# Kernel optimization log

Measured on AMD Instinct MI355X. Metric: run time of the kernel, lower is better.

Reference implementation:

```python
import jax, jax.numpy as jnp
import numpy as np

DIM = 768
HEADS = 12
HEAD_DIM = DIM // HEADS
MAX_LEN = 2048
EPS = 1e-5

def layer_norm(x, w, b):
    mu = jnp.mean(x, axis=-1, keepdims=True)
    var = jnp.var(x, axis=-1, keepdims=True)
    return (x - mu) * jax.lax.rsqrt(var + EPS) * w + b


def setup_inputs() -> dict:
    key = jax.random.key(0)
    ks = jax.random.split(key, 16)
    B, N = 2, 2048
    s = 1.0 / np.sqrt(DIM)
    inp = {
        "visible_features": jax.random.normal(ks[0], (B, N, DIM), jnp.float32),
        "infrared_features": jax.random.normal(ks[1], (B, N, DIM), jnp.float32),
        "wq": jax.random.normal(ks[2], (DIM, DIM), jnp.float32) * s,
        "bq": jnp.zeros((DIM,), jnp.float32),
        "lnq_w": jnp.ones((DIM,), jnp.float32),
        "lnq_b": jnp.zeros((DIM,), jnp.float32),
        "wk": jax.random.normal(ks[3], (DIM, DIM), jnp.float32) * s,
        "bk": jnp.zeros((DIM,), jnp.float32),
        "lnk_w": jnp.ones((DIM,), jnp.float32),
        "lnk_b": jnp.zeros((DIM,), jnp.float32),
        "wv": jax.random.normal(ks[4], (DIM, DIM), jnp.float32) * s,
        "bv": jnp.zeros((DIM,), jnp.float32),
        "lnv_w": jnp.ones((DIM,), jnp.float32),
        "lnv_b": jnp.zeros((DIM,), jnp.float32),
        "pos_emb": jax.random.normal(ks[5], (MAX_LEN, DIM), jnp.float32),
        "wo": jax.random.normal(ks[6], (DIM, DIM), jnp.float32) * s,
        "bo": jnp.zeros((DIM,), jnp.float32),
        "gate_w": jax.random.normal(ks[7], (DIM, 2 * DIM), jnp.float32) * (1.0 / np.sqrt(2 * DIM)),
        "gate_b": jnp.zeros((DIM,), jnp.float32),
        "ln_w": jnp.ones((DIM,), jnp.float32),
        "ln_b": jnp.zeros((DIM,), jnp.float32),
    }
    return inp


def reference(visible_features, infrared_features, wq, bq, lnq_w, lnq_b,
              wk, bk, lnk_w, lnk_b, wv, bv, lnv_w, lnv_b,
              pos_emb, wo, bo, gate_w, gate_b, ln_w, ln_b):
    B, N, _ = visible_features.shape
    scale = HEAD_DIM ** -0.5

    def proj_heads(x, w, b, gw, gb):
        y = layer_norm(x @ w.T + b, gw, gb)  # [B,N,D]
        return y.reshape(B, N, HEADS, HEAD_DIM).transpose(0, 2, 1, 3)  # [B,H,N,d]

    q = proj_heads(infrared_features, wq, bq, lnq_w, lnq_b)
    k = proj_heads(visible_features, wk, bk, lnk_w, lnk_b)
    v = proj_heads(visible_features, wv, bv, lnv_w, lnv_b)

    pos = pos_emb[:N].reshape(1, N, HEADS, HEAD_DIM).transpose(0, 2, 1, 3)  # [1,H,N,d]

    scores = jnp.einsum('bhnd,bhmd->bhnm', q, k) * scale
    scores = scores + jnp.einsum('bhnd,xhmd->bhnm', q, pos)
    attn = jax.nn.softmax(scores, axis=-1)  # dropout is identity in eval

    out = jnp.einsum('bhnm,bhmd->bhnd', attn, v)
    out = out.transpose(0, 2, 1, 3).reshape(B, N, DIM)
    out = out @ wo.T + bo

    gate = jax.nn.sigmoid(jnp.concatenate([visible_features, out], axis=-1) @ gate_w.T + gate_b)
    fused = visible_features * gate + out * (1.0 - gate)
    return layer_norm(fused, ln_w, ln_b)
```

## Files before the change

### kernel.cpp

```cpp
#include <hip/hip_runtime.h>
#include <hip/hip_bf16.h>

#define DIMC 768
#define NSEQ 2048
#define NB 2
#define NH 12
#define HD 64
#define EPSLN 1e-5f
#define LOG2E 1.44269504f

typedef __attribute__((ext_vector_type(8))) short          bf16x8;
typedef __attribute__((ext_vector_type(8))) unsigned short ushort8;
typedef __attribute__((ext_vector_type(4))) unsigned short ushort4v;
typedef __attribute__((ext_vector_type(4))) float          f32x4;
typedef __attribute__((ext_vector_type(2))) unsigned int   u32x2;
typedef unsigned int u32;

__device__ __forceinline__ unsigned short f2b(float f) {
    union { float f; unsigned u; } x; x.f = f;
    unsigned r = x.u + 0x7fffu + ((x.u >> 16) & 1u);
    return (unsigned short)(r >> 16);
}
__device__ __forceinline__ float b2f(unsigned short v) {
    union { unsigned u; float f; } x; x.u = ((u32)v) << 16; return x.f;
}

#define MFMA16(a, b, c) __builtin_amdgcn_mfma_f32_16x16x32_bf16((a), (b), (c), 0, 0, 0)

__device__ __forceinline__ void gl_lds16(const unsigned short* g, unsigned short* l) {
    __builtin_amdgcn_global_load_lds(
        (const __attribute__((address_space(1))) u32*)(const void*)g,
        (__attribute__((address_space(3))) u32*)(void*)l, 16, 0, 0);
}

#define G_WQ   147456
#define G_MW   442368
#define G_G2   147456
#define G_WO   147456
#define G_VIS  786432
#define G_INF  786432
#define G_BF_TOTAL (G_WQ + G_MW + G_G2 + G_WO + G_VIS + G_INF)
#define G_BIAS 576
#define G_ALL  (G_BF_TOTAL + G_BIAS)

__global__ __launch_bounds__(256)
void cast_all_kernel(const float* __restrict__ wq, const float* __restrict__ wk,
                     const float* __restrict__ wv, const float* __restrict__ gw,
                     const float* __restrict__ wo,
                     const float* __restrict__ bk, const float* __restrict__ bv,
                     const float* __restrict__ gb,
                     const float* __restrict__ vis, const float* __restrict__ inf_,
                     unsigned short* __restrict__ o_wq, unsigned short* __restrict__ o_mw,
                     unsigned short* __restrict__ o_g2, unsigned short* __restrict__ o_wo,
                     unsigned short* __restrict__ o_wot,
                     unsigned short* __restrict__ o_vis, unsigned short* __restrict__ o_inf,
                     float* __restrict__ o_biasc)
{
    const int g = blockIdx.x * 256 + threadIdx.x;
    if (g >= G_ALL) return;
    if (g >= G_BF_TOTAL) {
        const int e0 = (g - G_BF_TOTAL) * 4;
        float4 r;
        float* pr = (float*)&r;
        #pragma unroll
        for (int t = 0; t < 4; ++t) {
            const int e = e0 + t;
            pr[t] = (e < 768) ? bk[e] : (e < 1536) ? bv[e - 768] : gb[e - 1536];
        }
        *(float4*)&o_biasc[e0] = r;
        return;
    }
    const float* src; unsigned short* dst; int soff, doff = 0;
    bool is_wo = false; int wor = 0, woc = 0;
    int gg = g;
    if (gg < G_WQ) { src = wq; dst = o_wq; soff = gg; doff = gg; }
    else if ((gg -= G_WQ) < G_MW) {
        const int row = gg / 192, c4 = gg % 192;
        dst = o_mw; doff = gg;
        if      (row < 768)  { src = wk; soff = row * 192 + c4; }
        else if (row < 1536) { src = wv; soff = (row - 768) * 192 + c4; }
        else                 { src = gw; soff = (row - 1536) * 384 + c4; }
    }
    else if ((gg -= G_MW) < G_G2) {
        const int row = gg / 192, c4 = gg % 192;
        src = gw; soff = row * 384 + 192 + c4; dst = o_g2; doff = gg;
    }
    else if ((gg -= G_G2) < G_WO) {
        src = wo; dst = o_wo; soff = gg; doff = gg;
        is_wo = true; wor = gg / 192; woc = (gg % 192) * 4;
    }
    else if ((gg -= G_WO) < G_VIS) { src = vis;  dst = o_vis; soff = gg; doff = gg; }
    else { gg -= G_VIS;              src = inf_; dst = o_inf; soff = gg; doff = gg; }
    f32x4 v = ((const f32x4*)src)[soff];
    ushort4v t;
    t[0] = f2b(v[0]); t[1] = f2b(v[1]); t[2] = f2b(v[2]); t[3] = f2b(v[3]);
    ((ushort4v*)dst)[doff] = t;
    if (is_wo) {
        #pragma unroll
        for (int e = 0; e < 4; ++e)
            o_wot[(size_t)(woc + e) * DIMC + wor] = t[e];
    }
}

__global__ __launch_bounds__(256)
void bias2_kernel(const float* __restrict__ gw, const float* __restrict__ bo,
                  float* __restrict__ biasc2)
{
    const int i = blockIdx.x * 256 + threadIdx.x;
    if (i >= 768) return;
    biasc2[i] = bo[i];
    const float* row = gw + (size_t)i * 1536 + 768;
    float s = 0.f;
    for (int k = 0; k < 768; k += 4) {
        float4 gv = *(const float4*)&row[k];
        float4 bv = *(const float4*)&bo[k];
        s += gv.x * bv.x + gv.y * bv.y + gv.z * bv.z + gv.w * bv.w;
    }
    biasc2[768 + i] = s;
}

__device__ __forceinline__ void gemm_core128(const unsigned short* __restrict__ A,
                                             const unsigned short* __restrict__ W,
                                             int m0, int n0,
                                             unsigned short* As, unsigned short* Bs,
                                             f32x4 (&acc)[4][4])
{
    const int lane = threadIdx.x & 63, wid = threadIdx.x >> 6;
    const int wm = wid >> 1, wn = wid & 1;
    const int r16 = lane & 15, kg = lane >> 4;
    const int lr = lane >> 3, lc = (lane & 7) * 8;

    auto stage = [&](int k0, int buf) {
        #pragma unroll
        for (int i = 0; i < 4; ++i) {
            const int c = wid * 4 + i;
            gl_lds16(&A[(size_t)(m0 + c * 8 + lr) * DIMC + k0 + lc], &As[buf * 8192 + c * 512]);
            gl_lds16(&W[(size_t)(n0 + c * 8 + lr) * DIMC + k0 + lc], &Bs[buf * 8192 + c * 512]);
        }
    };

    stage(0, 0);
    for (int t = 0; t < 12; ++t) {
        const int cur = t & 1;
        if (t < 11) {
            stage((t + 1) * 64, cur ^ 1);
            asm volatile("s_waitcnt vmcnt(8)" ::: "memory");
        } else {
            asm volatile("s_waitcnt vmcnt(0)" ::: "memory");
        }
        __builtin_amdgcn_s_barrier();
        __builtin_amdgcn_sched_barrier(0);
        #pragma unroll
        for (int ks = 0; ks < 2; ++ks) {
            bf16x8 af[4], bg[4];
            #pragma unroll
            for (int mi = 0; mi < 4; ++mi)
                af[mi] = *(const bf16x8*)&As[cur * 8192 + (wm * 64 + mi * 16 + r16) * 64 + ks * 32 + kg * 8];
            #pragma unroll
            for (int nj = 0; nj < 4; ++nj)
                bg[nj] = *(const bf16x8*)&Bs[cur * 8192 + (wn * 64 + nj * 16 + r16) * 64 + ks * 32 + kg * 8];
            __builtin_amdgcn_s_setprio(1);
            #pragma unroll
            for (int mi = 0; mi < 4; ++mi)
                #pragma unroll
                for (int nj = 0; nj < 4; ++nj)
                    acc[mi][nj] = MFMA16(af[mi], bg[nj], acc[mi][nj]);
            __builtin_amdgcn_s_setprio(0);
        }
        __builtin_amdgcn_sched_barrier(0);
        __builtin_amdgcn_s_barrier();
    }
}

__global__ __launch_bounds__(256)
void gemm_p1(const unsigned short* __restrict__ inf_b, const unsigned short* __restrict__ vis_b,
             const unsigned short* __restrict__ g2_b,  const unsigned short* __restrict__ wq_b,
             const unsigned short* __restrict__ mw_b,  const unsigned short* __restrict__ wo_t,
             const float* __restrict__ bq, const float* __restrict__ biasc,
             unsigned short* __restrict__ qpre,
             unsigned short* __restrict__ k_b, unsigned short* __restrict__ v_b,
             float* __restrict__ Gd, unsigned short* __restrict__ W2)
{
    __shared__ unsigned short As[2 * 8192];
    __shared__ unsigned short Bs[2 * 8192];
    const int orig = (int)blockIdx.x;
    const int xcd = orig & 7, ix = orig >> 3;
    int bid = (xcd < 4 ? xcd * 101 : 404 + (xcd - 4) * 100) + ix;

    const unsigned short *A, *W;
    int m0, n0, sub;
    if (bid < 192)      { sub = 0; const int b = bid;       m0 = (b / 6)  * 128; n0 = (b % 6)  * 128; A = inf_b; W = wq_b; }
    else if (bid < 768) { sub = 1; const int b = bid - 192; m0 = (b / 18) * 128; n0 = (b % 18) * 128; A = vis_b; W = mw_b; }
    else                { sub = 2; const int b = bid - 768; m0 = (b / 6)  * 128; n0 = (b % 6)  * 128; A = g2_b;  W = wo_t; }

    f32x4 acc[4][4] = {};
    gemm_core128(A, W, m0, n0, As, Bs, acc);

    const int lane = threadIdx.x & 63, wid = threadIdx.x >> 6;
    const int wm = wid >> 1, wn = wid & 1;
    const int r16 = lane & 15, kg = lane >> 4;
    #pragma unroll
    for (int mi = 0; mi < 4; ++mi)
    #pragma unroll
    for (int nj = 0; nj < 4; ++nj) {
        const int gr0 = m0 + wm * 64 + mi * 16 + kg * 4;
        const int gc  = n0 + wn * 64 + nj * 16 + r16;
        #pragma unroll
        for (int r = 0; r < 4; ++r) {
            const int gr = gr0 + r;
            float val = acc[mi][nj][r];
            if (sub == 0) {
                qpre[(size_t)gr * DIMC + gc] = f2b(val + bq[gc]);
            } else if (sub == 1) {
                val += biasc[gc];
                if      (gc < 768)  k_b[(size_t)gr * DIMC + gc] = f2b(val);
                else if (gc < 1536) v_b[(size_t)gr * DIMC + (gc - 768)] = f2b(val);
                else                Gd[(size_t)gr * DIMC + (gc - 1536)] = val;
            } else {
                W2[(size_t)gr * DIMC + gc] = f2b(val);
            }
        }
    }
}

__global__ __launch_bounds__(256)
void gemm_p2(const unsigned short* __restrict__ ao_b, const unsigned short* __restrict__ wo_cat,
             const float* __restrict__ biasc2,
             float* __restrict__ Oc, float* __restrict__ Gd)
{
    __shared__ unsigned short As[2 * 8192];
    __shared__ unsigned short Bs[2 * 8192];
    int bid = (int)blockIdx.x;
    bid = (bid & 7) * 48 + (bid >> 3);
    const int m0 = (bid / 12) * 128, n0 = (bid % 12) * 128;

    f32x4 acc[4][4] = {};
    gemm_core128(ao_b, wo_cat, m0, n0, As, Bs, acc);

    const int lane = threadIdx.x & 63, wid = threadIdx.x >> 6;
    const int wm = wid >> 1, wn = wid & 1;
    const int r16 = lane & 15, kg = lane >> 4;
    #pragma unroll
    for (int mi = 0; mi < 4; ++mi)
    #pragma unroll
    for (int nj = 0; nj < 4; ++nj) {
        const int gr0 = m0 + wm * 64 + mi * 16 + kg * 4;
        const int gc  = n0 + wn * 64 + nj * 16 + r16;
        #pragma unroll
        for (int r = 0; r < 4; ++r) {
            const int gr = gr0 + r;
            const float val = acc[mi][nj][r] + biasc2[gc];
            if (gc < 768) Oc[(size_t)gr * DIMC + gc] = val;
            else          Gd[(size_t)gr * DIMC + (gc - 768)] += val;
        }
    }
}

__global__ __launch_bounds__(256)
void ln_all_kernel(const unsigned short* __restrict__ qpre,
                   const float* __restrict__ lnqw, const float* __restrict__ lnqb,
                   const float* __restrict__ lnkw, const float* __restrict__ lnkb,
                   const float* __restrict__ lnvw, const float* __restrict__ lnvb,
                   const float* __restrict__ pos,
                   unsigned short* __restrict__ q_b,
                   unsigned short* __restrict__ k_b, unsigned short* __restrict__ v_b)
{
    const int bid = blockIdx.x;
    const int mode = bid >> 12;
    const int row = bid & 4095;
    const int n = row & (NSEQ - 1);
    const unsigned short* src;
    unsigned short* dst;
    const float *w, *b;
    if (mode == 0)      { src = qpre + (size_t)row * DIMC; dst = q_b + (size_t)row * DIMC; w = lnqw; b = lnqb; }
    else if (mode == 1) { src = dst = k_b + (size_t)row * DIMC; w = lnkw; b = lnkb; }
    else                { src = dst = v_b + (size_t)row * DIMC; w = lnvw; b = lnvb; }

    float x[3];
    float s = 0.f, q = 0.f;
    #pragma unroll
    for (int u = 0; u < 3; ++u) {
        const int j = threadIdx.x + u * 256;
        x[u] = b2f(src[j]);
        s += x[u];
        q += x[u] * x[u];
    }
    #pragma unroll
    for (int off = 32; off > 0; off >>= 1) {
        s += __shfl_down(s, off);
        q += __shfl_down(q, off);
    }
    __shared__ float ls[8];
    const int wv_ = threadIdx.x >> 6;
    if ((threadIdx.x & 63) == 0) { ls[wv_] = s; ls[4 + wv_] = q; }
    __syncthreads();
    if (threadIdx.x == 0) {
        ls[0] = ls[0] + ls[1] + ls[2] + ls[3];
        ls[4] = ls[4] + ls[5] + ls[6] + ls[7];
    }
    __syncthreads();
    const float mu  = ls[0] * (1.f / DIMC);
    const float var = ls[4] * (1.f / DIMC) - mu * mu;
    const float rs  = rsqrtf(var + EPSLN);
    #pragma unroll
    for (int u = 0; u < 3; ++u) {
        const int j = threadIdx.x + u * 256;
        float y = (x[u] - mu) * rs * w[j] + b[j];
        if (mode == 1) y = y * (0.125f * LOG2E) + pos[(size_t)n * DIMC + j] * LOG2E;
        dst[j] = f2b(y);
    }
}

__global__ __launch_bounds__(256, 3)
void attn_bf16_kernel(const unsigned short* __restrict__ Q,
                      const unsigned short* __restrict__ K,
                      const unsigned short* __restrict__ V,
                      unsigned short* __restrict__ O)
{
    __shared__ unsigned short Ks[128][72];
    __shared__ unsigned short Vt[64][136];
    __shared__ unsigned short Ps[4][16][136];

    const int bh = blockIdx.x;
    const int b = bh / NH, h = bh % NH;
    const int n0 = blockIdx.y * 64;
    const int tid = threadIdx.x;
    const int lane = tid & 63, w = tid >> 6;
    const int r16 = lane & 15, kg = lane >> 4;

    const size_t base = (size_t)b * NSEQ * DIMC + (size_t)h * HD;

    const size_t qoff = base + (size_t)(n0 + w * 16 + r16) * DIMC + kg * 8;
    bf16x8 aq0 = *(const bf16x8*)&Q[qoff];
    bf16x8 aq1 = *(const bf16x8*)&Q[qoff + 32];

    const int krow = tid >> 1;
    const int kcol = (tid & 1) * 32;
    const unsigned short* Kg = K + base + (size_t)krow * DIMC + kcol;
    const int vkv = lane;
    const int vdc = w * 16;
    const unsigned short* Vg = V + base + (size_t)vkv * DIMC + vdc;

    f32x4 o[4] = {};
    float m_run = -1e30f, l_run = 0.f;

    ushort8 pk[4];
    ushort8 pv[2][2];

    auto pf_load = [&](size_t adv) {
        #pragma unroll
        for (int i = 0; i < 4; ++i) pk[i] = *(const ushort8*)(Kg + adv + 8 * i);
        #pragma unroll
        for (int rep = 0; rep < 2; ++rep)
            #pragma unroll
            for (int hh = 0; hh < 2; ++hh)
                pv[rep][hh] = *(const ushort8*)(Vg + adv + (size_t)rep * 64 * DIMC + hh * 8);
    };
    auto pf_write = [&]() {
        #pragma unroll
        for (int i = 0; i < 4; ++i) *(ushort8*)&Ks[krow][kcol + 8 * i] = pk[i];
        #pragma unroll
        for (int rep = 0; rep < 2; ++rep)
            #pragma unroll
            for (int hh = 0; hh < 2; ++hh)
                #pragma unroll
                for (int e = 0; e < 8; ++e)
                    Vt[vdc + hh * 8 + e][vkv + rep * 64] = pv[rep][hh][e];
    };

    pf_load(0);
    pf_write();
    __syncthreads();

    for (int m0 = 0; m0 < NSEQ; m0 += 128) {
        const bool more = (m0 + 128 < NSEQ);
        if (more) pf_load((size_t)(m0 + 128) * DIMC);
        __builtin_amdgcn_sched_barrier(0);

        f32x4 sv[8];
        #pragma unroll
        for (int f = 0; f < 8; ++f) sv[f] = (f32x4){0.f, 0.f, 0.f, 0.f};
        __builtin_amdgcn_s_setprio(1);
        #pragma unroll
        for (int f = 0; f < 8; ++f) {
            bf16x8 kb0 = *(const bf16x8*)&Ks[f * 16 + r16][kg * 8];
            bf16x8 kb1 = *(const bf16x8*)&Ks[f * 16 + r16][32 + kg * 8];
            sv[f] = MFMA16(kb0, aq0, sv[f]);
            sv[f] = MFMA16(kb1, aq1, sv[f]);
        }
        __builtin_amdgcn_s_setprio(0);

        float mf[8];
        #pragma unroll
        for (int f = 0; f < 8; ++f)
            mf[f] = fmaxf(fmaxf(sv[f][0], sv[f][1]), fmaxf(sv[f][2], sv[f][3]));
        float m01 = fmaxf(mf[0], mf[1]), m23 = fmaxf(mf[2], mf[3]);
        float m45 = fmaxf(mf[4], mf[5]), m67 = fmaxf(mf[6], mf[7]);
        float mt = fmaxf(fmaxf(m01, m23), fmaxf(m45, m67));
        mt = fmaxf(mt, __shfl_xor(mt, 16));
        mt = fmaxf(mt, __shfl_xor(mt, 32));

        const bool defer = __all(mt - m_run <= 8.0f);
        float corr = 1.f;
        if (!defer) {
            const float mn = fmaxf(m_run, mt);
            corr = exp2f(m_run - mn);
            m_run = mn;
        }

        float sf[8];
        #pragma unroll
        for (int f = 0; f < 8; ++f) {
            float p0 = exp2f(sv[f][0] - m_run);
            float p1 = exp2f(sv[f][1] - m_run);
            float p2 = exp2f(sv[f][2] - m_run);
            float p3 = exp2f(sv[f][3] - m_run);
            sf[f] = (p0 + p1) + (p2 + p3);
            u32 w0, w1;
            asm("v_cvt_pk_bf16_f32 %0, %1, %2" : "=v"(w0) : "v"(p0), "v"(p1));
            asm("v_cvt_pk_bf16_f32 %0, %1, %2" : "=v"(w1) : "v"(p2), "v"(p3));
            u32x2 pw; pw[0] = w0; pw[1] = w1;
            *(u32x2*)&Ps[w][r16][f * 16 + kg * 4] = pw;
        }
        float st = ((sf[0] + sf[1]) + (sf[2] + sf[3])) + ((sf[4] + sf[5]) + (sf[6] + sf[7]));
        st += __shfl_xor(st, 16);
        st += __shfl_xor(st, 32);
        l_run = l_run * corr + st;

        if (!defer) {
            #pragma unroll
            for (int jj = 0; jj < 4; ++jj) {
                const float cq = __shfl(corr, kg * 4 + jj);
                o[0][jj] *= cq; o[1][jj] *= cq; o[2][jj] *= cq; o[3][jj] *= cq;
            }
        }

        bf16x8 pa[4];
        #pragma unroll
        for (int s = 0; s < 4; ++s)
            pa[s] = *(const bf16x8*)&Ps[w][r16][s * 32 + kg * 8];
        __builtin_amdgcn_s_setprio(1);
        #pragma unroll
        for (int nj = 0; nj < 4; ++nj) {
            #pragma unroll
            for (int s = 0; s < 4; ++s) {
                bf16x8 vb = *(const bf16x8*)&Vt[nj * 16 + r16][s * 32 + kg * 8];
                o[nj] = MFMA16(pa[s], vb, o[nj]);
            }
        }
        __builtin_amdgcn_s_setprio(0);

        __builtin_amdgcn_s_barrier();
        __builtin_amdgcn_sched_barrier(0);
        if (more) pf_write();
        __syncthreads();
    }

    const float linv = 1.f / l_run;
    #pragma unroll
    for (int jj = 0; jj < 4; ++jj) {
        const float cq = __shfl(linv, kg * 4 + jj);
        #pragma unroll
        for (int nj = 0; nj < 4; ++nj) {
            const size_t go = base + (size_t)(n0 + w * 16 + kg * 4 + jj) * DIMC + nj * 16 + r16;
            O[go] = f2b(o[nj][jj] * cq);
        }
    }
}

__global__ __launch_bounds__(256)
void fuse_ln_kernel(const float* __restrict__ vis,
                    const float* __restrict__ Oc,
                    const float* __restrict__ G,
                    const float* __restrict__ w,
                    const float* __restrict__ b,
                    float* __restrict__ out)
{
    const int row = blockIdx.x;
    float f[3];
    float s = 0.f, q = 0.f;
    #pragma unroll
    for (int u = 0; u < 3; ++u) {
        const size_t idx = (size_t)row * DIMC + threadIdx.x + u * 256;
        const float vv = vis[idx];
        const float oo = Oc[idx];
        const float gg = 1.f / (1.f + __expf(-G[idx]));
        f[u] = vv * gg + oo * (1.f - gg);
        s += f[u];
        q += f[u] * f[u];
    }
    #pragma unroll
    for (int off = 32; off > 0; off >>= 1) {
        s += __shfl_down(s, off);
        q += __shfl_down(q, off);
    }
    __shared__ float ls[8];
    const int wv_ = threadIdx.x >> 6;
    if ((threadIdx.x & 63) == 0) { ls[wv_] = s; ls[4 + wv_] = q; }
    __syncthreads();
    if (threadIdx.x == 0) {
        ls[0] = ls[0] + ls[1] + ls[2] + ls[3];
        ls[4] = ls[4] + ls[5] + ls[6] + ls[7];
    }
    __syncthreads();
    const float mu  = ls[0] * (1.f / DIMC);
    const float var = ls[4] * (1.f / DIMC) - mu * mu;
    const float rs  = rsqrtf(var + EPSLN);
    #pragma unroll
    for (int u = 0; u < 3; ++u) {
        const int j = threadIdx.x + u * 256;
        out[(size_t)row * DIMC + j] = (f[u] - mu) * rs * w[j] + b[j];
    }
}

extern "C" void kernel_launch(void* const* d_in, const int* in_sizes, int n_in,
                              void* d_out, int out_size, void* d_ws, size_t ws_size,
                              hipStream_t stream)
{
    const float* vis  = (const float*)d_in[0];
    const float* inf_ = (const float*)d_in[1];
    const float* wq   = (const float*)d_in[2];
    const float* bq   = (const float*)d_in[3];
    const float* lnqw = (const float*)d_in[4];
    const float* lnqb = (const float*)d_in[5];
    const float* wk   = (const float*)d_in[6];
    const float* bk   = (const float*)d_in[7];
    const float* lnkw = (const float*)d_in[8];
    const float* lnkb = (const float*)d_in[9];
    const float* wv   = (const float*)d_in[10];
    const float* bv   = (const float*)d_in[11];
    const float* lnvw = (const float*)d_in[12];
    const float* lnvb = (const float*)d_in[13];
    const float* pos  = (const float*)d_in[14];
    const float* wo   = (const float*)d_in[15];
    const float* bo   = (const float*)d_in[16];
    const float* gw   = (const float*)d_in[17];
    const float* gb   = (const float*)d_in[18];
    const float* lnw  = (const float*)d_in[19];
    const float* lnb  = (const float*)d_in[20];

    const size_t WEL = 589824;
    const size_t MWEL = 1769472;
    const size_t BUF = (size_t)NB * NSEQ * DIMC;

    unsigned short* p = (unsigned short*)d_ws;
    unsigned short* wq_b   = p;  p += WEL;
    unsigned short* mw_b   = p;  p += MWEL;
    unsigned short* g2_b   = p;  p += WEL;
    unsigned short* wo_b   = p;  p += WEL;
    unsigned short* W2     = p;  p += WEL;
    unsigned short* wo_t   = p;  p += WEL;
    unsigned short* vis_b  = p;  p += BUF;
    unsigned short* inf_b  = p;  p += BUF;
    unsigned short* qpre_b = p;  p += BUF;
    unsigned short* q_b    = p;  p += BUF;
    unsigned short* k_b    = p;  p += BUF;
    unsigned short* v_b    = p;  p += BUF;
    float* biasc  = (float*)p;  p += 4608;
    float* biasc2 = (float*)p;  p += 3072;

    float* Gd = (float*)d_out;
    float* Oc = (float*)k_b;

    dim3 blk(256);

    bias2_kernel<<<dim3(3), blk, 0, stream>>>(gw, bo, biasc2);
    cast_all_kernel<<<dim3((G_ALL + 255) / 256), blk, 0, stream>>>(
        wq, wk, wv, gw, wo, bk, bv, gb, vis, inf_,
        wq_b, mw_b, g2_b, wo_b, wo_t, vis_b, inf_b, biasc);

    gemm_p1<<<dim3(804), blk, 0, stream>>>(inf_b, vis_b, g2_b, wq_b, mw_b, wo_t,
                                           bq, biasc, qpre_b, k_b, v_b, Gd, W2);

    ln_all_kernel<<<dim3(12288), blk, 0, stream>>>(qpre_b, lnqw, lnqb, lnkw, lnkb,
                                                   lnvw, lnvb, pos, q_b, k_b, v_b);

    attn_bf16_kernel<<<dim3(NB * NH, NSEQ / 64), blk, 0, stream>>>(q_b, k_b, v_b, q_b);

    gemm_p2<<<dim3(384), blk, 0, stream>>>(q_b, wo_b, biasc2, Oc, Gd);

    fuse_ln_kernel<<<dim3(4096), blk, 0, stream>>>(vis, Oc, Gd, lnw, lnb, (float*)d_out);
}
```

Baseline: 338.3 us.

## Replace precomputed Wo·G2 weight fold with sequential Wo then gate GEMMs

```diff
diff --git a/kernel.cpp b/kernel.cpp
--- a/kernel.cpp
+++ b/kernel.cpp
@@ -52,7 +52,6 @@
                      const float* __restrict__ vis, const float* __restrict__ inf_,
                      unsigned short* __restrict__ o_wq, unsigned short* __restrict__ o_mw,
                      unsigned short* __restrict__ o_g2, unsigned short* __restrict__ o_wo,
-                     unsigned short* __restrict__ o_wot,
                      unsigned short* __restrict__ o_vis, unsigned short* __restrict__ o_inf,
                      float* __restrict__ o_biasc)
 {
@@ -71,7 +70,6 @@
         return;
     }
     const float* src; unsigned short* dst; int soff, doff = 0;
-    bool is_wo = false; int wor = 0, woc = 0;
     int gg = g;
     if (gg < G_WQ) { src = wq; dst = o_wq; soff = gg; doff = gg; }
     else if ((gg -= G_WQ) < G_MW) {
@@ -85,45 +83,20 @@
         const int row = gg / 192, c4 = gg % 192;
         src = gw; soff = row * 384 + 192 + c4; dst = o_g2; doff = gg;
     }
-    else if ((gg -= G_G2) < G_WO) {
-        src = wo; dst = o_wo; soff = gg; doff = gg;
-        is_wo = true; wor = gg / 192; woc = (gg % 192) * 4;
-    }
+    else if ((gg -= G_G2) < G_WO)  { src = wo;   dst = o_wo;  soff = gg; doff = gg; }
     else if ((gg -= G_WO) < G_VIS) { src = vis;  dst = o_vis; soff = gg; doff = gg; }
     else { gg -= G_VIS;              src = inf_; dst = o_inf; soff = gg; doff = gg; }
     f32x4 v = ((const f32x4*)src)[soff];
     ushort4v t;
     t[0] = f2b(v[0]); t[1] = f2b(v[1]); t[2] = f2b(v[2]); t[3] = f2b(v[3]);
     ((ushort4v*)dst)[doff] = t;
-    if (is_wo) {
-        #pragma unroll
-        for (int e = 0; e < 4; ++e)
-            o_wot[(size_t)(woc + e) * DIMC + wor] = t[e];
-    }
-}
-
-__global__ __launch_bounds__(256)
-void bias2_kernel(const float* __restrict__ gw, const float* __restrict__ bo,
-                  float* __restrict__ biasc2)
-{
-    const int i = blockIdx.x * 256 + threadIdx.x;
-    if (i >= 768) return;
-    biasc2[i] = bo[i];
-    const float* row = gw + (size_t)i * 1536 + 768;
-    float s = 0.f;
-    for (int k = 0; k < 768; k += 4) {
-        float4 gv = *(const float4*)&row[k];
-        float4 bv = *(const float4*)&bo[k];
-        s += gv.x * bv.x + gv.y * bv.y + gv.z * bv.z + gv.w * bv.w;
-    }
-    biasc2[768 + i] = s;
-}
-
-__device__ __forceinline__ void gemm_core128(const unsigned short* __restrict__ A,
-                                             const unsigned short* __restrict__ W,
-                                             int m0, int n0,
-                                             unsigned short* As, unsigned short* Bs,
-                                             f32x4 (&acc)[4][4])
+}
+
+__device__ __forceinline__ void gemm_core(const unsigned short* __restrict__ A,
+                                          const unsigned short* __restrict__ W,
+                                          int m0, int n0,
+                                          unsigned short* As, unsigned short* Bs,
+                                          f32x4 (&acc)[4][2])
 {
     const int lane = threadIdx.x & 63, wid = threadIdx.x >> 6;
     const int wm = wid >> 1, wn = wid & 1;
@@ -135,7 +108,11 @@
         for (int i = 0; i < 4; ++i) {
             const int c = wid * 4 + i;
             gl_lds16(&A[(size_t)(m0 + c * 8 + lr) * DIMC + k0 + lc], &As[buf * 8192 + c * 512]);
-            gl_lds16(&W[(size_t)(n0 + c * 8 + lr) * DIMC + k0 + lc], &Bs[buf * 8192 + c * 512]);
+        }
+        #pragma unroll
+        for (int i = 0; i < 2; ++i) {
+            const int c = wid * 2 + i;
+            gl_lds16(&W[(size_t)(n0 + c * 8 + lr) * DIMC + k0 + lc], &Bs[buf * 4096 + c * 512]);
         }
     };
 
@@ -144,7 +121,7 @@
         const int cur = t & 1;
         if (t < 11) {
             stage((t + 1) * 64, cur ^ 1);
-            asm volatile("s_waitcnt vmcnt(8)" ::: "memory");
+            asm volatile("s_waitcnt vmcnt(6)" ::: "memory");
         } else {
             asm volatile("s_waitcnt vmcnt(0)" ::: "memory");
         }
@@ -152,18 +129,18 @@
         __builtin_amdgcn_sched_barrier(0);
         #pragma unroll
         for (int ks = 0; ks < 2; ++ks) {
-            bf16x8 af[4], bg[4];
+            bf16x8 af[4], bg[2];
             #pragma unroll
             for (int mi = 0; mi < 4; ++mi)
                 af[mi] = *(const bf16x8*)&As[cur * 8192 + (wm * 64 + mi * 16 + r16) * 64 + ks * 32 + kg * 8];
             #pragma unroll
-            for (int nj = 0; nj < 4; ++nj)
-                bg[nj] = *(const bf16x8*)&Bs[cur * 8192 + (wn * 64 + nj * 16 + r16) * 64 + ks * 32 + kg * 8];
+            for (int nj = 0; nj < 2; ++nj)
+                bg[nj] = *(const bf16x8*)&Bs[cur * 4096 + (wn * 32 + nj * 16 + r16) * 64 + ks * 32 + kg * 8];
             __builtin_amdgcn_s_setprio(1);
             #pragma unroll
             for (int mi = 0; mi < 4; ++mi)
                 #pragma unroll
-                for (int nj = 0; nj < 4; ++nj)
+                for (int nj = 0; nj < 2; ++nj)
                     acc[mi][nj] = MFMA16(af[mi], bg[nj], acc[mi][nj]);
             __builtin_amdgcn_s_setprio(0);
         }
@@ -174,27 +151,22 @@
 
 __global__ __launch_bounds__(256)
 void gemm_p1(const unsigned short* __restrict__ inf_b, const unsigned short* __restrict__ vis_b,
-             const unsigned short* __restrict__ g2_b,  const unsigned short* __restrict__ wq_b,
-             const unsigned short* __restrict__ mw_b,  const unsigned short* __restrict__ wo_t,
+             const unsigned short* __restrict__ wq_b,  const unsigned short* __restrict__ mw_b,
              const float* __restrict__ bq, const float* __restrict__ biasc,
              unsigned short* __restrict__ qpre,
              unsigned short* __restrict__ k_b, unsigned short* __restrict__ v_b,
-             float* __restrict__ Gd, unsigned short* __restrict__ W2)
+             float* __restrict__ Gd)
 {
     __shared__ unsigned short As[2 * 8192];
-    __shared__ unsigned short Bs[2 * 8192];
-    const int orig = (int)blockIdx.x;
-    const int xcd = orig & 7, ix = orig >> 3;
-    int bid = (xcd < 4 ? xcd * 101 : 404 + (xcd - 4) * 100) + ix;
-
+    __shared__ unsigned short Bs[2 * 4096];
+    const int bid = (int)blockIdx.x;
     const unsigned short *A, *W;
     int m0, n0, sub;
-    if (bid < 192)      { sub = 0; const int b = bid;       m0 = (b / 6)  * 128; n0 = (b % 6)  * 128; A = inf_b; W = wq_b; }
-    else if (bid < 768) { sub = 1; const int b = bid - 192; m0 = (b / 18) * 128; n0 = (b % 18) * 128; A = vis_b; W = mw_b; }
-    else                { sub = 2; const int b = bid - 768; m0 = (b / 6)  * 128; n0 = (b % 6)  * 128; A = g2_b;  W = wo_t; }
-
-    f32x4 acc[4][4] = {};
-    gemm_core128(A, W, m0, n0, As, Bs, acc);
+    if (bid < 384) { sub = 0; const int b = bid;       m0 = (b / 12) * 128; n0 = (b % 12) * 64; A = inf_b; W = wq_b; }
+    else           { sub = 1; const int b = bid - 384; m0 = (b / 36) * 128; n0 = (b % 36) * 64; A = vis_b; W = mw_b; }
+
+    f32x4 acc[4][2] = {};
+    gemm_core(A, W, m0, n0, As, Bs, acc);
 
     const int lane = threadIdx.x & 63, wid = threadIdx.x >> 6;
     const int wm = wid >> 1, wn = wid & 1;
@@ -202,40 +174,37 @@
     #pragma unroll
     for (int mi = 0; mi < 4; ++mi)
     #pragma unroll
-    for (int nj = 0; nj < 4; ++nj) {
+    for (int nj = 0; nj < 2; ++nj) {
         const int gr0 = m0 + wm * 64 + mi * 16 + kg * 4;
-        const int gc  = n0 + wn * 64 + nj * 16 + r16;
+        const int gc  = n0 + wn * 32 + nj * 16 + r16;
         #pragma unroll
         for (int r = 0; r < 4; ++r) {
             const int gr = gr0 + r;
             float val = acc[mi][nj][r];
             if (sub == 0) {
                 qpre[(size_t)gr * DIMC + gc] = f2b(val + bq[gc]);
-            } else if (sub == 1) {
+            } else {
                 val += biasc[gc];
                 if      (gc < 768)  k_b[(size_t)gr * DIMC + gc] = f2b(val);
                 else if (gc < 1536) v_b[(size_t)gr * DIMC + (gc - 768)] = f2b(val);
                 else                Gd[(size_t)gr * DIMC + (gc - 1536)] = val;
-            } else {
-                W2[(size_t)gr * DIMC + gc] = f2b(val);
             }
         }
     }
 }
 
 __global__ __launch_bounds__(256)
-void gemm_p2(const unsigned short* __restrict__ ao_b, const unsigned short* __restrict__ wo_cat,
-             const float* __restrict__ biasc2,
-             float* __restrict__ Oc, float* __restrict__ Gd)
+void gemm_wo(const unsigned short* __restrict__ ao_b, const unsigned short* __restrict__ wo_b,
+             const float* __restrict__ bo,
+             float* __restrict__ Oc, unsigned short* __restrict__ oc_b)
 {
     __shared__ unsigned short As[2 * 8192];
-    __shared__ unsigned short Bs[2 * 8192];
-    int bid = (int)blockIdx.x;
-    bid = (bid & 7) * 48 + (bid >> 3);
-    const int m0 = (bid / 12) * 128, n0 = (bid % 12) * 128;
-
-    f32x4 acc[4][4] = {};
-    gemm_core128(ao_b, wo_cat, m0, n0, As, Bs, acc);
+    __shared__ unsigned short Bs[2 * 4096];
+    const int bid = (int)blockIdx.x;
+    const int m0 = (bid / 12) * 128, n0 = (bid % 12) * 64;
+
+    f32x4 acc[4][2] = {};
+    gemm_core(ao_b, wo_b, m0, n0, As, Bs, acc);
 
     const int lane = threadIdx.x & 63, wid = threadIdx.x >> 6;
     const int wm = wid >> 1, wn = wid & 1;
@@ -243,16 +212,43 @@
     #pragma unroll
     for (int mi = 0; mi < 4; ++mi)
     #pragma unroll
-    for (int nj = 0; nj < 4; ++nj) {
+    for (int nj = 0; nj < 2; ++nj) {
         const int gr0 = m0 + wm * 64 + mi * 16 + kg * 4;
-        const int gc  = n0 + wn * 64 + nj * 16 + r16;
+        const int gc  = n0 + wn * 32 + nj * 16 + r16;
         #pragma unroll
         for (int r = 0; r < 4; ++r) {
-            const int gr = gr0 + r;
-            const float val = acc[mi][nj][r] + biasc2[gc];
-            if (gc < 768) Oc[(size_t)gr * DIMC + gc] = val;
-            else          Gd[(size_t)gr * DIMC + (gc - 768)] += val;
-        }
+            const size_t idx = (size_t)(gr0 + r) * DIMC + gc;
+            const float val = acc[mi][nj][r] + bo[gc];
+            Oc[idx] = val;
+            oc_b[idx] = f2b(val);
+        }
+    }
+}
+
+__global__ __launch_bounds__(256)
+void gemm_g2(const unsigned short* __restrict__ oc_b, const unsigned short* __restrict__ g2_b,
+             float* __restrict__ Gd)
+{
+    __shared__ unsigned short As[2 * 8192];
+    __shared__ unsigned short Bs[2 * 4096];
+    const int bid = (int)blockIdx.x;
+    const int m0 = (bid / 12) * 128, n0 = (bid % 12) * 64;
+
+    f32x4 acc[4][2] = {};
+    gemm_core(oc_b, g2_b, m0, n0, As, Bs, acc);
+
+    const int lane = threadIdx.x & 63, wid = threadIdx.x >> 6;
+    const int wm = wid >> 1, wn = wid & 1;
+    const int r16 = lane & 15, kg = lane >> 4;
+    #pragma unroll
+    for (int mi = 0; mi < 4; ++mi)
+    #pragma unroll
+    for (int nj = 0; nj < 2; ++nj) {
+        const int gr0 = m0 + wm * 64 + mi * 16 + kg * 4;
+        const int gc  = n0 + wn * 32 + nj * 16 + r16;
+        #pragma unroll
+        for (int r = 0; r < 4; ++r)
+            Gd[(size_t)(gr0 + r) * DIMC + gc] += acc[mi][nj][r];
     }
 }
 
@@ -548,36 +544,35 @@
     unsigned short* mw_b   = p;  p += MWEL;
     unsigned short* g2_b   = p;  p += WEL;
     unsigned short* wo_b   = p;  p += WEL;
-    unsigned short* W2     = p;  p += WEL;
-    unsigned short* wo_t   = p;  p += WEL;
     unsigned short* vis_b  = p;  p += BUF;
     unsigned short* inf_b  = p;  p += BUF;
     unsigned short* qpre_b = p;  p += BUF;
     unsigned short* q_b    = p;  p += BUF;
     unsigned short* k_b    = p;  p += BUF;
     unsigned short* v_b    = p;  p += BUF;
-    float* biasc  = (float*)p;  p += 4608;
-    float* biasc2 = (float*)p;  p += 3072;
+    float* biasc = (float*)p;   p += 4608;
 
     float* Gd = (float*)d_out;
     float* Oc = (float*)k_b;
+    unsigned short* oc_b = qpre_b;
 
     dim3 blk(256);
 
-    bias2_kernel<<<dim3(3), blk, 0, stream>>>(gw, bo, biasc2);
     cast_all_kernel<<<dim3((G_ALL + 255) / 256), blk, 0, stream>>>(
         wq, wk, wv, gw, wo, bk, bv, gb, vis, inf_,
-        wq_b, mw_b, g2_b, wo_b, wo_t, vis_b, inf_b, biasc);
-
-    gemm_p1<<<dim3(804), blk, 0, stream>>>(inf_b, vis_b, g2_b, wq_b, mw_b, wo_t,
-                                           bq, biasc, qpre_b, k_b, v_b, Gd, W2);
+        wq_b, mw_b, g2_b, wo_b, vis_b, inf_b, biasc);
+
+    gemm_p1<<<dim3(1536), blk, 0, stream>>>(inf_b, vis_b, wq_b, mw_b,
+                                            bq, biasc, qpre_b, k_b, v_b, Gd);
 
     ln_all_kernel<<<dim3(12288), blk, 0, stream>>>(qpre_b, lnqw, lnqb, lnkw, lnkb,
                                                    lnvw, lnvb, pos, q_b, k_b, v_b);
 
     attn_bf16_kernel<<<dim3(NB * NH, NSEQ / 64), blk, 0, stream>>>(q_b, k_b, v_b, q_b);
 
-    gemm_p2<<<dim3(384), blk, 0, stream>>>(q_b, wo_b, biasc2, Oc, Gd);
+    gemm_wo<<<dim3(384), blk, 0, stream>>>(q_b, wo_b, bo, Oc, oc_b);
+
+    gemm_g2<<<dim3(384), blk, 0, stream>>>(oc_b, g2_b, Gd);
 
     fuse_ln_kernel<<<dim3(4096), blk, 0, stream>>>(vis, Oc, Gd, lnw, lnb, (float*)d_out);
 }
```

Result: faster. 297.2 us (-12.1%).
